# Kernel optimization log

Hardware: AMD Instinct MI355X
Metric: run time of the kernel (lower is better)

## Reference

```python
import jax, jax.numpy as jnp
import numpy as np

H = 3.0        # args.h smoothing length
N_NODES = 100000
DIM_HIDDEN = 128
D = 3


def setup_inputs() -> dict:
    key = jax.random.key(0)
    ks = jax.random.split(key, 10)
    E = 1600000
    v = jax.random.normal(ks[0], (N_NODES, D), dtype=jnp.float32)
    r_ij = jax.random.normal(ks[1], (E, D), dtype=jnp.float32)
    edge_index = jax.random.randint(ks[2], (2, E), 0, N_NODES, dtype=jnp.int64)
    # teacher MLP params: [1+D] -> dim_hidden -> dim_hidden -> 1
    def lin(k, fan_in, fan_out):
        bound = 1.0 / np.sqrt(fan_in)
        kw, kb = jax.random.split(k)
        W = jax.random.uniform(kw, (fan_out, fan_in), jnp.float32, -bound, bound)
        b = jax.random.uniform(kb, (fan_out,), jnp.float32, -bound, bound)
        return W, b
    W0, b0 = lin(ks[3], 1 + D, DIM_HIDDEN)
    W1, b1 = lin(ks[4], DIM_HIDDEN, DIM_HIDDEN)
    W2, b2 = lin(ks[5], DIM_HIDDEN, 1)
    return {"v": v, "r_ij": r_ij, "W0": W0, "b0": b0, "W1": W1, "b1": b1,
            "W2": W2, "b2": b2, "edge_index": edge_index}


def _teacher(x, W0, b0, W1, b1, W2, b2):
    x = jax.nn.silu(x @ W0.T + b0)
    x = jax.nn.silu(x @ W1.T + b1)
    return x @ W2.T + b2  # [E, 1]


def _scatter_mean(x, idx, n):
    s = jax.ops.segment_sum(x, idx, num_segments=n)
    c = jax.ops.segment_sum(jnp.ones((idx.shape[0], 1), x.dtype), idx, num_segments=n)
    return s / jnp.maximum(c, 1.0)


def reference(v, r_ij, W0, b0, W1, b1, W2, b2, edge_index):
    i = edge_index[0]
    j = edge_index[1]
    v_ij = v[i] - v[j]                                   # [E, D] gather-diff
    r_ = jnp.sqrt(jnp.sum(r_ij * r_ij, axis=-1, keepdims=True)) / H  # [E, 1]
    m_i = _teacher(jnp.concatenate([r_, v_ij], axis=-1), W0, b0, W1, b1, W2, b2)
    m_j = _teacher(jnp.concatenate([r_, -v_ij], axis=-1), W0, b0, W1, b1, W2, b2)
    S = _scatter_mean(m_i, i, N_NODES) + _scatter_mean(m_j, j, N_NODES)  # [N, 1]
    return S
```

## Files before the change

### kernel.cpp

```cpp
#include <hip/hip_runtime.h>

typedef unsigned short ushort_t;
typedef __bf16 bf16x8 __attribute__((ext_vector_type(8)));
typedef __bf16 bf16x2 __attribute__((ext_vector_type(2)));
typedef float f32x4 __attribute__((ext_vector_type(4)));

__device__ __forceinline__ ushort_t f2bf(float f) {
    unsigned u;
    __builtin_memcpy(&u, &f, 4);
    u += 0x7fffu + ((u >> 16) & 1u);
    return (ushort_t)(u >> 16);
}

__device__ __forceinline__ float silu(float x) {
    float e = __builtin_amdgcn_exp2f(x * -1.442695040888963f);
    return x * __builtin_amdgcn_rcpf(1.0f + e);
}

__device__ __forceinline__ float rdlane(float v, int l) {
    return __builtin_bit_cast(float, __builtin_amdgcn_readlane(__builtin_bit_cast(int, v), l));
}


#define CNT_UNIT 65536.0

__global__ __launch_bounds__(256, 2) void mlp_kernel(
    const float* __restrict__ v,
    const float* __restrict__ rij,
    const float* __restrict__ W0,
    const float* __restrict__ b0,
    const float* __restrict__ W1,
    const float* __restrict__ b1,
    const float* __restrict__ W2,
    const float* __restrict__ b2,
    const int* __restrict__ eidx,
    double* __restrict__ acc_i, double* __restrict__ acc_j,
    int E, int nchunks)
{
    __shared__ ushort_t sW1[16384];
    __shared__ ushort_t sH0[16384];

    const int tid  = threadIdx.x;
    const int lane = tid & 63;
    const int wave = tid >> 6;

    {
        int n = tid >> 1, half = tid & 1;
        const float* src = W1 + n * 128;
#pragma unroll
        for (int dk = 0; dk < 8; dk++) {
            int k0   = half * 64 + dk * 8;
            int frag = (n >> 4) * 4 + (k0 >> 5);
            int slot = (n & 15) + 16 * ((k0 >> 3) & 3);
            ushort_t tmp[8];
#pragma unroll
            for (int t = 0; t < 8; t++) tmp[t] = f2bf(src[k0 + t]);
            *(uint4*)(&sW1[frag * 512 + slot * 8]) = *(const uint4*)tmp;
        }
    }

    float4 w0q[2]; float b0v[2];
#pragma unroll
    for (int kk = 0; kk < 2; kk++) {
        int h = 2 * lane + kk;
        w0q[kk].x = W0[h * 4 + 0];
        w0q[kk].y = W0[h * 4 + 1];
        w0q[kk].z = W0[h * 4 + 2];
        w0q[kk].w = W0[h * 4 + 3];
        b0v[kk]   = b0[h];
    }
    float b1v[8], w2v[8];
#pragma unroll
    for (int nt = 0; nt < 8; nt++) {
        int ccol = nt * 16 + (lane & 15);
        b1v[nt] = b1[ccol];
        w2v[nt] = W2[ccol];
    }
    const float b2f = b2[0];

    __syncthreads();

    const int q = lane >> 4, c = lane & 15, p = (lane >> 2) & 3, bsub = lane & 3;
    const int ple  = lane >> 2;
    const int comp = lane & 3;

    auto preload = [&](int ch, float& val_o, int& idx_o) {
        float val = 0.f; int idxr = 0;
        int pe = ch * 64 + wave * 16 + ple;
        if (ch < nchunks && pe < E) {
            if (comp == 3) {
                float r0 = rij[3 * pe], r1 = rij[3 * pe + 1], r2 = rij[3 * pe + 2];
                val = sqrtf(fmaf(r0, r0, fmaf(r1, r1, r2 * r2))) * (1.0f / 3.0f);
            } else {
                int i = eidx[pe], jj = eidx[E + pe];
                idxr = (comp == 1) ? jj : i;
                val = v[3 * i + comp] - v[3 * jj + comp];
            }
        }
        val_o = val; idx_o = idxr;
    };

    float val; int idxr;
    preload(blockIdx.x, val, idxr);

    for (int chunk = blockIdx.x; chunk < nchunks; chunk += gridDim.x) {
        const float val_cur = val;
        const int   idx_cur = idxr;
        preload(chunk + (int)gridDim.x, val, idxr);

        const int ebase = chunk * 64 + wave * 16;

#pragma unroll
        for (int le = 0; le < 16; le++) {
            float vx = rdlane(val_cur, le * 4 + 0);
            float vy = rdlane(val_cur, le * 4 + 1);
            float vz = rdlane(val_cur, le * 4 + 2);
            float rr = rdlane(val_cur, le * 4 + 3);
            float si[2], sj[2];
#pragma unroll
            for (int kk = 0; kk < 2; kk++) {
                float cc = fmaf(w0q[kk].x, rr, b0v[kk]);
                float dd = fmaf(w0q[kk].y, vx, fmaf(w0q[kk].z, vy, w0q[kk].w * vz));
                si[kk] = silu(cc + dd);
                sj[kk] = silu(cc - dd);
            }
            bf16x2 pki, pkj;
            pki[0] = (__bf16)si[0]; pki[1] = (__bf16)si[1];
            pkj[0] = (__bf16)sj[0]; pkj[1] = (__bf16)sj[1];
            int mi = wave * 32 + 2 * le;
            int fr_i = ((mi >> 4) << 2) + q;
            int fr_j = (((mi + 1) >> 4) << 2) + q;
            int sl_i = (((mi & 15) ^ q ^ (p << 2)) & 15) + (p << 4);
            int sl_j = ((((mi + 1) & 15) ^ q ^ (p << 2)) & 15) + (p << 4);
            ((unsigned*)sH0)[fr_i * 256 + sl_i * 4 + bsub] = __builtin_bit_cast(unsigned, pki);
            ((unsigned*)sH0)[fr_j * 256 + sl_j * 4 + bsub] = __builtin_bit_cast(unsigned, pkj);
        }

        f32x4 acc[2][8];
#pragma unroll
        for (int t = 0; t < 2; t++)
#pragma unroll
            for (int nt = 0; nt < 8; nt++)
                acc[t][nt] = (f32x4){0.f, 0.f, 0.f, 0.f};

#pragma unroll
        for (int ks = 0; ks < 4; ks++) {
            int sl_rd = (((lane & 15) ^ ks ^ (q << 2)) & 15) + 16 * q;
            bf16x8 a0 = *(const bf16x8*)(&sH0[((2 * wave + 0) * 4 + ks) * 512 + sl_rd * 8]);
            bf16x8 a1 = *(const bf16x8*)(&sH0[((2 * wave + 1) * 4 + ks) * 512 + sl_rd * 8]);
#pragma unroll
            for (int nt = 0; nt < 8; nt++) {
                bf16x8 bb = *(const bf16x8*)(&sW1[(nt * 4 + ks) * 512 + lane * 8]);
                acc[0][nt] = __builtin_amdgcn_mfma_f32_16x16x32_bf16(a0, bb, acc[0][nt], 0, 0, 0);
                acc[1][nt] = __builtin_amdgcn_mfma_f32_16x16x32_bf16(a1, bb, acc[1][nt], 0, 0, 0);
            }
        }

        float rs[2][4] = {{0.f, 0.f, 0.f, 0.f}, {0.f, 0.f, 0.f, 0.f}};
#pragma unroll
        for (int t = 0; t < 2; t++)
#pragma unroll
            for (int nt = 0; nt < 8; nt++)
#pragma unroll
                for (int r = 0; r < 4; r++) {
                    float x = acc[t][nt][r] + b1v[nt];
                    rs[t][r] = fmaf(silu(x), w2v[nt], rs[t][r]);
                }
#pragma unroll
        for (int t = 0; t < 2; t++)
#pragma unroll
            for (int r = 0; r < 4; r++) {
                float s = rs[t][r];
                s += __shfl_xor(s, 1, 64);
                s += __shfl_xor(s, 2, 64);
                s += __shfl_xor(s, 4, 64);
                s += __shfl_xor(s, 8, 64);
                int el  = t * 8 + q * 2 + (r >> 1);
                int src = el * 4 + (r & 1);
                int node = __shfl(idx_cur, src, 64);
                int e = ebase + el;
                if (c == 0 && e < E) {
                    double contrib = (double)(s + b2f) + CNT_UNIT;
                    if (r & 1) atomicAdd(&acc_j[node], contrib);
                    else       atomicAdd(&acc_i[node], contrib);
                }
            }
    }
}

__global__ void finalize_kernel(const double* __restrict__ acc_i,
                                const double* __restrict__ acc_j,
                                float* __restrict__ out, int N)
{
    int n = blockIdx.x * 256 + threadIdx.x;
    if (n < N) {
        double ti = acc_i[n], tj = acc_j[n];
        double ci = rint(ti * (1.0 / CNT_UNIT));
        double cj = rint(tj * (1.0 / CNT_UNIT));
        double si = ti - ci * CNT_UNIT;
        double sj = tj - cj * CNT_UNIT;
        out[n] = (float)(si / fmax(ci, 1.0) + sj / fmax(cj, 1.0));
    }
}

extern "C" void kernel_launch(void* const* d_in, const int* in_sizes, int n_in,
                              void* d_out, int out_size, void* d_ws, size_t ws_size,
                              hipStream_t stream) {
    const float* v   = (const float*)d_in[0];
    const float* rij = (const float*)d_in[1];
    const float* W0  = (const float*)d_in[2];
    const float* b0  = (const float*)d_in[3];
    const float* W1  = (const float*)d_in[4];
    const float* b1  = (const float*)d_in[5];
    const float* W2  = (const float*)d_in[6];
    const float* b2  = (const float*)d_in[7];
    const int* eidx  = (const int*)d_in[8];

    const int E = in_sizes[1] / 3;
    const int N = out_size;

    double* acc_i = (double*)d_ws;
    double* acc_j = acc_i + N;

    hipMemsetAsync(d_ws, 0, (size_t)2 * N * sizeof(double), stream);

    int nchunks = (E + 63) / 64;
    int grid = nchunks < 512 ? nchunks : 512;
    mlp_kernel<<<grid, 256, 0, stream>>>(v, rij, W0, b0, W1, b1, W2, b2, eidx,
                                         acc_i, acc_j, E, nchunks);
    finalize_kernel<<<(N + 255) / 256, 256, 0, stream>>>(acc_i, acc_j,
                                                         (float*)d_out, N);
}
```

Measured before the change: 424.8 us.

## Use 512-thread blocks with 8 edges per wave to halve accumulator registers

Blocks grow from 256 to 512 threads, and each wave now handles 8 edges (one 16-row MFMA tile) per chunk instead of 16. Each wave therefore keeps 8 accumulator tiles instead of 16, which cuts register pressure so that launch bounds of 4 blocks per CU can be met. The b1 bias is folded into the accumulator initialisation. The cost is that only half the lanes do preload gathers, and each sW1 fragment load now feeds one MFMA instead of two, which raises the ratio of LDS traffic to math.

```diff
diff --git a/kernel.cpp b/kernel.cpp
--- a/kernel.cpp
+++ b/kernel.cpp
@@ -24,7 +24,7 @@
 
 #define CNT_UNIT 65536.0
 
-__global__ __launch_bounds__(256, 2) void mlp_kernel(
+__global__ __launch_bounds__(512, 4) void mlp_kernel(
     const float* __restrict__ v,
     const float* __restrict__ rij,
     const float* __restrict__ W0,
@@ -45,11 +45,11 @@
     const int wave = tid >> 6;
 
     {
-        int n = tid >> 1, half = tid & 1;
+        int n = tid >> 2, qt = tid & 3;
         const float* src = W1 + n * 128;
 #pragma unroll
-        for (int dk = 0; dk < 8; dk++) {
-            int k0   = half * 64 + dk * 8;
+        for (int dk = 0; dk < 4; dk++) {
+            int k0   = qt * 32 + dk * 8;
             int frag = (n >> 4) * 4 + (k0 >> 5);
             int slot = (n & 15) + 16 * ((k0 >> 3) & 3);
             ushort_t tmp[8];
@@ -86,15 +86,17 @@
 
     auto preload = [&](int ch, float& val_o, int& idx_o) {
         float val = 0.f; int idxr = 0;
-        int pe = ch * 64 + wave * 16 + ple;
-        if (ch < nchunks && pe < E) {
-            if (comp == 3) {
-                float r0 = rij[3 * pe], r1 = rij[3 * pe + 1], r2 = rij[3 * pe + 2];
-                val = sqrtf(fmaf(r0, r0, fmaf(r1, r1, r2 * r2))) * (1.0f / 3.0f);
-            } else {
-                int i = eidx[pe], jj = eidx[E + pe];
-                idxr = (comp == 1) ? jj : i;
-                val = v[3 * i + comp] - v[3 * jj + comp];
+        if (ch < nchunks && lane < 32) {
+            int pe = ch * 64 + wave * 8 + ple;
+            if (pe < E) {
+                if (comp == 3) {
+                    float r0 = rij[3 * pe], r1 = rij[3 * pe + 1], r2 = rij[3 * pe + 2];
+                    val = sqrtf(fmaf(r0, r0, fmaf(r1, r1, r2 * r2))) * (1.0f / 3.0f);
+                } else {
+                    int i = eidx[pe], jj = eidx[E + pe];
+                    idxr = (comp == 1) ? jj : i;
+                    val = v[3 * i + comp] - v[3 * jj + comp];
+                }
             }
         }
         val_o = val; idx_o = idxr;
@@ -108,10 +110,10 @@
         const int   idx_cur = idxr;
         preload(chunk + (int)gridDim.x, val, idxr);
 
-        const int ebase = chunk * 64 + wave * 16;
-
-#pragma unroll
-        for (int le = 0; le < 16; le++) {
+        const int ebase = chunk * 64 + wave * 8;
+
+#pragma unroll
+        for (int le = 0; le < 8; le++) {
             float vx = rdlane(val_cur, le * 4 + 0);
             float vy = rdlane(val_cur, le * 4 + 1);
             float vz = rdlane(val_cur, le * 4 + 2);
@@ -127,64 +129,54 @@
             bf16x2 pki, pkj;
             pki[0] = (__bf16)si[0]; pki[1] = (__bf16)si[1];
             pkj[0] = (__bf16)sj[0]; pkj[1] = (__bf16)sj[1];
-            int mi = wave * 32 + 2 * le;
-            int fr_i = ((mi >> 4) << 2) + q;
-            int fr_j = (((mi + 1) >> 4) << 2) + q;
-            int sl_i = (((mi & 15) ^ q ^ (p << 2)) & 15) + (p << 4);
-            int sl_j = ((((mi + 1) & 15) ^ q ^ (p << 2)) & 15) + (p << 4);
-            ((unsigned*)sH0)[fr_i * 256 + sl_i * 4 + bsub] = __builtin_bit_cast(unsigned, pki);
-            ((unsigned*)sH0)[fr_j * 256 + sl_j * 4 + bsub] = __builtin_bit_cast(unsigned, pkj);
-        }
-
-        f32x4 acc[2][8];
-#pragma unroll
-        for (int t = 0; t < 2; t++)
-#pragma unroll
-            for (int nt = 0; nt < 8; nt++)
-                acc[t][nt] = (f32x4){0.f, 0.f, 0.f, 0.f};
+            int mi = 2 * le;
+            int fr   = wave * 4 + q;
+            int sl_i = ((mi ^ q ^ (p << 2)) & 15) + (p << 4);
+            int sl_j = (((mi + 1) ^ q ^ (p << 2)) & 15) + (p << 4);
+            ((unsigned*)sH0)[fr * 256 + sl_i * 4 + bsub] = __builtin_bit_cast(unsigned, pki);
+            ((unsigned*)sH0)[fr * 256 + sl_j * 4 + bsub] = __builtin_bit_cast(unsigned, pkj);
+        }
+
+        f32x4 acc[8];
+#pragma unroll
+        for (int nt = 0; nt < 8; nt++)
+            acc[nt] = (f32x4){b1v[nt], b1v[nt], b1v[nt], b1v[nt]};
 
 #pragma unroll
         for (int ks = 0; ks < 4; ks++) {
             int sl_rd = (((lane & 15) ^ ks ^ (q << 2)) & 15) + 16 * q;
-            bf16x8 a0 = *(const bf16x8*)(&sH0[((2 * wave + 0) * 4 + ks) * 512 + sl_rd * 8]);
-            bf16x8 a1 = *(const bf16x8*)(&sH0[((2 * wave + 1) * 4 + ks) * 512 + sl_rd * 8]);
+            bf16x8 a0 = *(const bf16x8*)(&sH0[(wave * 4 + ks) * 512 + sl_rd * 8]);
 #pragma unroll
             for (int nt = 0; nt < 8; nt++) {
                 bf16x8 bb = *(const bf16x8*)(&sW1[(nt * 4 + ks) * 512 + lane * 8]);
-                acc[0][nt] = __builtin_amdgcn_mfma_f32_16x16x32_bf16(a0, bb, acc[0][nt], 0, 0, 0);
-                acc[1][nt] = __builtin_amdgcn_mfma_f32_16x16x32_bf16(a1, bb, acc[1][nt], 0, 0, 0);
-            }
-        }
-
-        float rs[2][4] = {{0.f, 0.f, 0.f, 0.f}, {0.f, 0.f, 0.f, 0.f}};
-#pragma unroll
-        for (int t = 0; t < 2; t++)
-#pragma unroll
-            for (int nt = 0; nt < 8; nt++)
-#pragma unroll
-                for (int r = 0; r < 4; r++) {
-                    float x = acc[t][nt][r] + b1v[nt];
-                    rs[t][r] = fmaf(silu(x), w2v[nt], rs[t][r]);
-                }
-#pragma unroll
-        for (int t = 0; t < 2; t++)
-#pragma unroll
-            for (int r = 0; r < 4; r++) {
-                float s = rs[t][r];
-                s += __shfl_xor(s, 1, 64);
-                s += __shfl_xor(s, 2, 64);
-                s += __shfl_xor(s, 4, 64);
-                s += __shfl_xor(s, 8, 64);
-                int el  = t * 8 + q * 2 + (r >> 1);
-                int src = el * 4 + (r & 1);
-                int node = __shfl(idx_cur, src, 64);
-                int e = ebase + el;
-                if (c == 0 && e < E) {
-                    double contrib = (double)(s + b2f) + CNT_UNIT;
-                    if (r & 1) atomicAdd(&acc_j[node], contrib);
-                    else       atomicAdd(&acc_i[node], contrib);
-                }
-            }
+                acc[nt] = __builtin_amdgcn_mfma_f32_16x16x32_bf16(a0, bb, acc[nt], 0, 0, 0);
+            }
+        }
+
+        float rs[4] = {0.f, 0.f, 0.f, 0.f};
+#pragma unroll
+        for (int nt = 0; nt < 8; nt++)
+#pragma unroll
+            for (int r = 0; r < 4; r++)
+                rs[r] = fmaf(silu(acc[nt][r]), w2v[nt], rs[r]);
+
+#pragma unroll
+        for (int r = 0; r < 4; r++) {
+            float s = rs[r];
+            s += __shfl_xor(s, 1, 64);
+            s += __shfl_xor(s, 2, 64);
+            s += __shfl_xor(s, 4, 64);
+            s += __shfl_xor(s, 8, 64);
+            int el  = q * 2 + (r >> 1);
+            int src = el * 4 + (r & 1);
+            int node = __shfl(idx_cur, src, 64);
+            int e = ebase + el;
+            if (c == 0 && e < E) {
+                double contrib = (double)(s + b2f) + CNT_UNIT;
+                if (r & 1) atomicAdd(&acc_j[node], contrib);
+                else       atomicAdd(&acc_i[node], contrib);
+            }
+        }
     }
 }
 
@@ -226,7 +218,7 @@
 
     int nchunks = (E + 63) / 64;
     int grid = nchunks < 512 ? nchunks : 512;
-    mlp_kernel<<<grid, 256, 0, stream>>>(v, rij, W0, b0, W1, b1, W2, b2, eidx,
+    mlp_kernel<<<grid, 512, 0, stream>>>(v, rij, W0, b0, W1, b1, W2, b2, eidx,
                                          acc_i, acc_j, E, nchunks);
     finalize_kernel<<<(N + 255) / 256, 256, 0, stream>>>(acc_i, acc_j,
                                                          (float*)d_out, N);
```

After: 1.120 ms. 2.64x slower.

## Read W1 fragments from global memory, halve LDS, and double grid size

Applied to the files above, without the earlier changes.

Moves the bf16 conversion and fragment layout of W1 into a separate one-block prep kernel that writes to workspace. The MLP kernel then reads W1 fragments straight from global memory (through cache) rather than from LDS, which halves shared memory per block and drops the startup barrier so more blocks can be resident; the grid is doubled to match. It also folds the -log2(e) factor into W0/b0 and seeds the accumulators with b1 to remove a few multiplies and adds. The cost is that every MFMA B-operand now comes from a global/L2 load instead of LDS, which may add latency to the inner loop.

```diff
diff --git a/kernel.cpp b/kernel.cpp
--- a/kernel.cpp
+++ b/kernel.cpp
@@ -12,6 +12,12 @@
     return (ushort_t)(u >> 16);
 }
 
+__device__ __forceinline__ float silu_t(float t) {
+    float e = __builtin_amdgcn_exp2f(t);
+    float x = t * -0.6931471805599453f;
+    return x * __builtin_amdgcn_rcpf(1.0f + e);
+}
+
 __device__ __forceinline__ float silu(float x) {
     float e = __builtin_amdgcn_exp2f(x * -1.442695040888963f);
     return x * __builtin_amdgcn_rcpf(1.0f + e);
@@ -23,13 +29,30 @@
 
 
 #define CNT_UNIT 65536.0
+
+
+__global__ void prep_w1(const float* __restrict__ W1, ushort_t* __restrict__ w1s) {
+    int tid = threadIdx.x;
+    int n = tid >> 1, half = tid & 1;
+    const float* src = W1 + n * 128;
+#pragma unroll
+    for (int dk = 0; dk < 8; dk++) {
+        int k0   = half * 64 + dk * 8;
+        int frag = (n >> 4) * 4 + (k0 >> 5);
+        int slot = (n & 15) + 16 * ((k0 >> 3) & 3);
+        ushort_t tmp[8];
+#pragma unroll
+        for (int t = 0; t < 8; t++) tmp[t] = f2bf(src[k0 + t]);
+        *(uint4*)(&w1s[frag * 512 + slot * 8]) = *(const uint4*)tmp;
+    }
+}
 
 __global__ __launch_bounds__(256, 2) void mlp_kernel(
     const float* __restrict__ v,
     const float* __restrict__ rij,
     const float* __restrict__ W0,
     const float* __restrict__ b0,
-    const float* __restrict__ W1,
+    const ushort_t* __restrict__ w1s,
     const float* __restrict__ b1,
     const float* __restrict__ W2,
     const float* __restrict__ b2,
@@ -37,37 +60,22 @@
     double* __restrict__ acc_i, double* __restrict__ acc_j,
     int E, int nchunks)
 {
-    __shared__ ushort_t sW1[16384];
     __shared__ ushort_t sH0[16384];
 
     const int tid  = threadIdx.x;
     const int lane = tid & 63;
     const int wave = tid >> 6;
 
-    {
-        int n = tid >> 1, half = tid & 1;
-        const float* src = W1 + n * 128;
-#pragma unroll
-        for (int dk = 0; dk < 8; dk++) {
-            int k0   = half * 64 + dk * 8;
-            int frag = (n >> 4) * 4 + (k0 >> 5);
-            int slot = (n & 15) + 16 * ((k0 >> 3) & 3);
-            ushort_t tmp[8];
-#pragma unroll
-            for (int t = 0; t < 8; t++) tmp[t] = f2bf(src[k0 + t]);
-            *(uint4*)(&sW1[frag * 512 + slot * 8]) = *(const uint4*)tmp;
-        }
-    }
-
+    const float KL2 = -1.442695040888963f;
     float4 w0q[2]; float b0v[2];
 #pragma unroll
     for (int kk = 0; kk < 2; kk++) {
         int h = 2 * lane + kk;
-        w0q[kk].x = W0[h * 4 + 0];
-        w0q[kk].y = W0[h * 4 + 1];
-        w0q[kk].z = W0[h * 4 + 2];
-        w0q[kk].w = W0[h * 4 + 3];
-        b0v[kk]   = b0[h];
+        w0q[kk].x = W0[h * 4 + 0] * KL2;
+        w0q[kk].y = W0[h * 4 + 1] * KL2;
+        w0q[kk].z = W0[h * 4 + 2] * KL2;
+        w0q[kk].w = W0[h * 4 + 3] * KL2;
+        b0v[kk]   = b0[h] * KL2;
     }
     float b1v[8], w2v[8];
 #pragma unroll
@@ -77,8 +85,6 @@
         w2v[nt] = W2[ccol];
     }
     const float b2f = b2[0];
-
-    __syncthreads();
 
     const int q = lane >> 4, c = lane & 15, p = (lane >> 2) & 3, bsub = lane & 3;
     const int ple  = lane >> 2;
@@ -121,19 +127,18 @@
             for (int kk = 0; kk < 2; kk++) {
                 float cc = fmaf(w0q[kk].x, rr, b0v[kk]);
                 float dd = fmaf(w0q[kk].y, vx, fmaf(w0q[kk].z, vy, w0q[kk].w * vz));
-                si[kk] = silu(cc + dd);
-                sj[kk] = silu(cc - dd);
+                si[kk] = silu_t(cc + dd);
+                sj[kk] = silu_t(cc - dd);
             }
             bf16x2 pki, pkj;
             pki[0] = (__bf16)si[0]; pki[1] = (__bf16)si[1];
             pkj[0] = (__bf16)sj[0]; pkj[1] = (__bf16)sj[1];
-            int mi = wave * 32 + 2 * le;
-            int fr_i = ((mi >> 4) << 2) + q;
-            int fr_j = (((mi + 1) >> 4) << 2) + q;
+            int mi = 2 * le;
+            int fr   = ((mi >> 4) << 2) + q;
             int sl_i = (((mi & 15) ^ q ^ (p << 2)) & 15) + (p << 4);
             int sl_j = ((((mi + 1) & 15) ^ q ^ (p << 2)) & 15) + (p << 4);
-            ((unsigned*)sH0)[fr_i * 256 + sl_i * 4 + bsub] = __builtin_bit_cast(unsigned, pki);
-            ((unsigned*)sH0)[fr_j * 256 + sl_j * 4 + bsub] = __builtin_bit_cast(unsigned, pkj);
+            ((unsigned*)sH0)[wave * 2048 + fr * 256 + sl_i * 4 + bsub] = __builtin_bit_cast(unsigned, pki);
+            ((unsigned*)sH0)[wave * 2048 + fr * 256 + sl_j * 4 + bsub] = __builtin_bit_cast(unsigned, pkj);
         }
 
         f32x4 acc[2][8];
@@ -141,16 +146,16 @@
         for (int t = 0; t < 2; t++)
 #pragma unroll
             for (int nt = 0; nt < 8; nt++)
-                acc[t][nt] = (f32x4){0.f, 0.f, 0.f, 0.f};
+                acc[t][nt] = (f32x4){b1v[nt], b1v[nt], b1v[nt], b1v[nt]};
 
 #pragma unroll
         for (int ks = 0; ks < 4; ks++) {
             int sl_rd = (((lane & 15) ^ ks ^ (q << 2)) & 15) + 16 * q;
-            bf16x8 a0 = *(const bf16x8*)(&sH0[((2 * wave + 0) * 4 + ks) * 512 + sl_rd * 8]);
-            bf16x8 a1 = *(const bf16x8*)(&sH0[((2 * wave + 1) * 4 + ks) * 512 + sl_rd * 8]);
+            bf16x8 a0 = *(const bf16x8*)(&sH0[wave * 4096 + (0 * 4 + ks) * 512 + sl_rd * 8]);
+            bf16x8 a1 = *(const bf16x8*)(&sH0[wave * 4096 + (1 * 4 + ks) * 512 + sl_rd * 8]);
 #pragma unroll
             for (int nt = 0; nt < 8; nt++) {
-                bf16x8 bb = *(const bf16x8*)(&sW1[(nt * 4 + ks) * 512 + lane * 8]);
+                bf16x8 bb = *(const bf16x8*)(&w1s[(nt * 4 + ks) * 512 + lane * 8]);
                 acc[0][nt] = __builtin_amdgcn_mfma_f32_16x16x32_bf16(a0, bb, acc[0][nt], 0, 0, 0);
                 acc[1][nt] = __builtin_amdgcn_mfma_f32_16x16x32_bf16(a1, bb, acc[1][nt], 0, 0, 0);
             }
@@ -162,10 +167,9 @@
 #pragma unroll
             for (int nt = 0; nt < 8; nt++)
 #pragma unroll
-                for (int r = 0; r < 4; r++) {
-                    float x = acc[t][nt][r] + b1v[nt];
-                    rs[t][r] = fmaf(silu(x), w2v[nt], rs[t][r]);
-                }
+                for (int r = 0; r < 4; r++)
+                    rs[t][r] = fmaf(silu(acc[t][nt][r]), w2v[nt], rs[t][r]);
+
 #pragma unroll
         for (int t = 0; t < 2; t++)
 #pragma unroll
@@ -221,12 +225,14 @@
 
     double* acc_i = (double*)d_ws;
     double* acc_j = acc_i + N;
+    ushort_t* w1s = (ushort_t*)(acc_j + N);
 
     hipMemsetAsync(d_ws, 0, (size_t)2 * N * sizeof(double), stream);
+    prep_w1<<<1, 256, 0, stream>>>(W1, w1s);
 
     int nchunks = (E + 63) / 64;
-    int grid = nchunks < 512 ? nchunks : 512;
-    mlp_kernel<<<grid, 256, 0, stream>>>(v, rij, W0, b0, W1, b1, W2, b2, eidx,
+    int grid = nchunks < 1024 ? nchunks : 1024;
+    mlp_kernel<<<grid, 256, 0, stream>>>(v, rij, W0, b0, w1s, b1, W2, b2, eidx,
                                          acc_i, acc_j, E, nchunks);
     finalize_kernel<<<(N + 255) / 256, 256, 0, stream>>>(acc_i, acc_j,
                                                          (float*)d_out, N);
```

Result: slower. 820.5 us (+93.2%).
